# Optimization experiments

Hardware: AMD Instinct MI355X
Metric: run time of the kernel (lower is better)

Reference implementation:

```python
import jax, jax.numpy as jnp
import numpy as np

N_MAPS = 6          # n: maps per class (5 kernels + 1 text)
N_CLASSES = 2       # len(text_classify)
RATIO = 3
LAMBDA = 0.7
EPS = 1e-4
NEG_INF = -1e30


def setup_inputs() -> dict:
    key = jax.random.key(0)
    k1, k2, k3 = jax.random.split(key, 3)
    B, C, H, W = 8, N_CLASSES * N_MAPS, 640, 640
    outputs = jax.random.normal(k1, (B, C, H, W), dtype=jnp.float32)
    labels = jax.random.uniform(k2, (B, C, H, W), dtype=jnp.float32)
    training_mask = jax.random.uniform(k3, (B, 1, H, W), dtype=jnp.float32)
    return {"outputs": outputs, "labels": labels, "training_mask": training_mask}


def _dice_loss(pred, target, mask):
    # pred/target: (B, HW) or (B, K, HW); mask broadcastable. sums over last axis.
    p = jax.nn.sigmoid(pred) * mask
    t = target * mask
    a = jnp.sum(p * t, axis=-1)
    b = jnp.sum(p * p, axis=-1) + EPS
    c = jnp.sum(t * t, axis=-1) + EPS
    return 1.0 - 2.0 * a / (b + c)


def _ohem_single(score, gt, tm):
    # score/gt/tm: (H, W). Returns float32 (H, W) selection mask.
    pos_num = jnp.sum((gt > 0.5) & (tm > 0.5))
    neg = gt <= 0.5
    neg_total = jnp.sum(neg)
    neg_num = jnp.minimum(pos_num * RATIO, neg_total)
    # descending sort of negative-position scores
    neg_sorted = -jnp.sort(-jnp.where(neg, score, NEG_INF).ravel())
    thr = neg_sorted[jnp.clip(neg_num - 1, 0, score.size - 1)]
    sel = ((score >= thr) | (gt > 0.5)) & (tm > 0.5)
    fallback = (pos_num == 0) | (neg_num == 0)
    return jnp.where(fallback, tm, sel.astype(jnp.float32))


def reference(outputs, labels, training_mask):
    B, C, H, W = outputs.shape
    tm = training_mask[:, 0]  # (B, H, W)
    text_losses, kernel_losses, class_losses = [], [], []
    for i in range(N_CLASSES):
        texts = outputs[:, (i + 1) * N_MAPS - 1]                 # (B, H, W)
        kernels = outputs[:, i * N_MAPS:(i + 1) * N_MAPS - 1]    # (B, K, H, W)
        gt_texts = labels[:, (i + 1) * N_MAPS - 1]
        gt_kernels = labels[:, i * N_MAPS:(i + 1) * N_MAPS - 1]
        # OHEM mask (detached in original via numpy round-trip)
        sel_text = jax.lax.stop_gradient(jax.vmap(_ohem_single)(texts, gt_texts, tm))
        loss_text = _dice_loss(texts.reshape(B, -1), gt_texts.reshape(B, -1),
                               sel_text.reshape(B, -1))  # (B,)
        # kernel mask: (sigmoid(texts) > 0.5) & (tm > 0.5), detached
        sel_k = jax.lax.stop_gradient(
            ((jax.nn.sigmoid(texts) > 0.5) & (tm > 0.5)).astype(jnp.float32))
        K = gt_kernels.shape[1]
        loss_kernels = _dice_loss(kernels.reshape(B, K, -1),
                                  gt_kernels.reshape(B, K, -1),
                                  sel_k.reshape(B, 1, -1))  # (B, K) per-kernel losses
        loss_kernels = jnp.mean(loss_kernels, axis=1)  # mean over kernels -> (B,)
        lt = jnp.mean(loss_text)      # reduction='mean'
        lk = jnp.mean(loss_kernels)
        loss = LAMBDA * lt + (1.0 - LAMBDA) * lk
        text_losses.append(lt)
        kernel_losses.append(lk)
        class_losses.append(loss)
    muti_class_loss_avg = jnp.mean(jnp.stack(class_losses))
    text_loss_avg = jnp.mean(jnp.stack(text_losses))
    kernel_loss_avg = jnp.mean(jnp.stack(kernel_losses))
    # stacked as (3,): [muti_class_loss_avg, text_loss_avg, kernel_loss_avg]
    return jnp.stack([muti_class_loss_avg, text_loss_avg, kernel_loss_avg])
```

## Files before the change

### kernel.cpp

```cpp
#include <hip/hip_runtime.h>

#define HW 409600
#define NCH 12

#define OFF_TACC   0
#define OFF_KACC   256
#define OFF_POS    2048
#define OFF_NEG    2112
#define OFF_DONE   2176
#define OFF_FB     2240
#define OFF_NEGNUM 2304
#define OFF_MAXNK  2368
#define OFF_SEL1   2432
#define OFF_KREM1  2496
#define OFF_SEL2   2560
#define OFF_KREM2  2624
#define OFF_THR    2688
#define OFF_HA     4096
#define OFF_HB     (OFF_HA + 16*2048*4)
#define OFF_HC     (OFF_HB + 16*2048*4)
#define OFF_META_END (OFF_HC + 16*1024*4)
#define OFF_MASK   ((OFF_META_END + 255) & ~255)

__device__ __forceinline__ unsigned flipkey(float x){
  unsigned b = __float_as_uint(x);
  return (b & 0x80000000u) ? ~b : (b | 0x80000000u);
}
__device__ __forceinline__ float unflip(unsigned u){
  unsigned b = (u & 0x80000000u) ? (u ^ 0x80000000u) : ~u;
  return __uint_as_float(b);
}

__global__ __launch_bounds__(256) void k_count(
    const float* __restrict__ outputs, const float* __restrict__ labels,
    const float* __restrict__ tmask, unsigned char* __restrict__ maskb,
    unsigned* __restrict__ posA, unsigned* __restrict__ negA,
    unsigned* __restrict__ maxnkA)
{
  int img = blockIdx.x / 100;
  int blk = blockIdx.x % 100;
  int ci = img >> 3, bi = img & 7;
  const float* tp = outputs + (size_t)(bi*NCH + ci*6 + 5)*HW;
  const float* gp = labels  + (size_t)(bi*NCH + ci*6 + 5)*HW;
  const float* mp = tmask   + (size_t)bi*HW;
  int base = blk*4096 + (int)threadIdx.x*4;

  float4 tv0 = *(const float4*)(tp+base);
  float4 tv1 = *(const float4*)(tp+base+1024);
  float4 tv2 = *(const float4*)(tp+base+2048);
  float4 tv3 = *(const float4*)(tp+base+3072);
  float4 gv0 = *(const float4*)(gp+base);
  float4 gv1 = *(const float4*)(gp+base+1024);
  float4 gv2 = *(const float4*)(gp+base+2048);
  float4 gv3 = *(const float4*)(gp+base+3072);
  float4 mv0 = *(const float4*)(mp+base);
  float4 mv1 = *(const float4*)(mp+base+1024);
  float4 mv2 = *(const float4*)(mp+base+2048);
  float4 mv3 = *(const float4*)(mp+base+3072);

  float tt[16]={tv0.x,tv0.y,tv0.z,tv0.w, tv1.x,tv1.y,tv1.z,tv1.w,
                tv2.x,tv2.y,tv2.z,tv2.w, tv3.x,tv3.y,tv3.z,tv3.w};
  float gg[16]={gv0.x,gv0.y,gv0.z,gv0.w, gv1.x,gv1.y,gv1.z,gv1.w,
                gv2.x,gv2.y,gv2.z,gv2.w, gv3.x,gv3.y,gv3.z,gv3.w};
  float mm[16]={mv0.x,mv0.y,mv0.z,mv0.w, mv1.x,mv1.y,mv1.z,mv1.w,
                mv2.x,mv2.y,mv2.z,mv2.w, mv3.x,mv3.y,mv3.z,mv3.w};

  unsigned pos=0, neg=0, mn=0xFFFFFFFFu;
  unsigned char mb[16];
  #pragma unroll
  for (int c=0;c<16;c++){
    bool isneg = (gg[c] <= 0.5f);
    bool tpos  = (mm[c] > 0.5f);
    pos += (unsigned)((!isneg) && tpos);
    neg += (unsigned)isneg;
    mb[c] = (unsigned char)((((tt[c] > 0.0f) && tpos) ? 1u : 0u) |
                            (tpos ? 2u : 0u) | (isneg ? 4u : 0u));
    if (isneg){ unsigned k = flipkey(tt[c]); mn = (k<mn)?k:mn; }
  }
  unsigned char* mw = maskb + (size_t)img*HW + base;
  *(uchar4*)(mw)      = make_uchar4(mb[0],mb[1],mb[2],mb[3]);
  *(uchar4*)(mw+1024) = make_uchar4(mb[4],mb[5],mb[6],mb[7]);
  *(uchar4*)(mw+2048) = make_uchar4(mb[8],mb[9],mb[10],mb[11]);
  *(uchar4*)(mw+3072) = make_uchar4(mb[12],mb[13],mb[14],mb[15]);

  #pragma unroll
  for (int o=32;o;o>>=1){
    pos += __shfl_down(pos,o,64);
    neg += __shfl_down(neg,o,64);
    unsigned om = __shfl_down(mn,o,64); mn = (om<mn)?om:mn;
  }
  __shared__ unsigned sp[4], sn[4], sm[4];
  int wv = threadIdx.x >> 6, ln = threadIdx.x & 63;
  if (ln==0){ sp[wv]=pos; sn[wv]=neg; sm[wv]=mn; }
  __syncthreads();
  if (threadIdx.x==0){
    unsigned m01 = (sm[0]<sm[1])?sm[0]:sm[1];
    unsigned m23 = (sm[2]<sm[3])?sm[2]:sm[3];
    unsigned m = (m01<m23)?m01:m23;
    atomicAdd(&posA[img], sp[0]+sp[1]+sp[2]+sp[3]);
    atomicAdd(&negA[img], sn[0]+sn[1]+sn[2]+sn[3]);
    atomicMax(&maxnkA[img], ~m);
  }
}

__global__ void k_decide(
    const unsigned* __restrict__ posA, const unsigned* __restrict__ negA,
    const unsigned* __restrict__ maxnkA, unsigned* __restrict__ doneA,
    unsigned* __restrict__ fbA, unsigned* __restrict__ negnumA,
    float* __restrict__ thrA)
{
  int img = threadIdx.x;
  if (img >= 16) return;
  unsigned pos = posA[img], negt = negA[img];
  unsigned p3 = pos*3u;
  unsigned negnum = (p3 < negt) ? p3 : negt;
  if (pos==0u || negnum==0u){
    doneA[img]=1u; fbA[img]=1u; negnumA[img]=1u; thrA[img]=0.0f;
  } else if (negnum == negt){
    doneA[img]=1u; fbA[img]=0u; negnumA[img]=negnum;
    thrA[img] = unflip(~maxnkA[img]);
  } else {
    doneA[img]=0u; fbA[img]=0u; negnumA[img]=negnum; thrA[img]=0.0f;
  }
}


__global__ __launch_bounds__(256) void k_hista(
    const float* __restrict__ outputs, const unsigned char* __restrict__ maskb,
    const unsigned* __restrict__ doneA, unsigned* __restrict__ histA)
{
  int img = blockIdx.x / 50;
  if (doneA[img]) return;
  int blk = blockIdx.x % 50;
  int ci = img>>3, bi = img&7;
  const float* tp = outputs + (size_t)(bi*NCH + ci*6 + 5)*HW;
  const unsigned char* mk = maskb + (size_t)img*HW;
  __shared__ unsigned lh[2048];
  for (int j=threadIdx.x; j<2048; j+=256) lh[j]=0u;
  __syncthreads();
  #pragma unroll
  for (int it=0; it<8; it++){
    int px = blk*8192 + it*1024 + (int)threadIdx.x*4;
    float4 tv = *(const float4*)(tp+px);
    uchar4 mq = *(const uchar4*)(mk+px);
    float tt[4]={tv.x,tv.y,tv.z,tv.w};
    unsigned char ma[4]={mq.x,mq.y,mq.z,mq.w};
    #pragma unroll
    for (int c=0;c<4;c++)
      if (ma[c] & 4) atomicAdd(&lh[flipkey(tt[c]) >> 21], 1u);
  }
  __syncthreads();
  unsigned* gh = histA + (size_t)img*2048u;
  for (int j=threadIdx.x; j<2048; j+=256){
    unsigned v = lh[j];
    if (v) atomicAdd(&gh[j], v);
  }
}

template<int NB>
__device__ void scan_desc(const unsigned* h, unsigned k, unsigned* selOut, unsigned* kremOut)
{
  const int PER = NB/256;
  int t = threadIdx.x;
  unsigned s=0;
  #pragma unroll
  for (int j=0;j<PER;j++) s += h[t*PER+j];
  __shared__ unsigned cs[256];
  cs[t]=s; __syncthreads();
  if (t==0){
    unsigned cum=0, ch=0, kin=k;
    for (int c=255;c>=0;c--){
      if (cum + cs[c] >= k){ ch=(unsigned)c; kin=k-cum; break; }
      cum += cs[c];
    }
    unsigned cum2=0, sel=ch*PER, kr=1;
    for (int x=PER-1;x>=0;x--){
      unsigned v = h[ch*PER+x];
      cum2 += v;
      if (cum2 >= kin){ sel=ch*PER+(unsigned)x; kr = kin - (cum2 - v); break; }
    }
    *selOut = sel; *kremOut = kr;
  }
}

__global__ __launch_bounds__(256) void k_scan_a(
    const unsigned* __restrict__ histA, const unsigned* __restrict__ doneA,
    const unsigned* __restrict__ negnumA, unsigned* __restrict__ sel1A,
    unsigned* __restrict__ krem1A)
{
  int img = blockIdx.x;
  if (doneA[img]) return;
  scan_desc<2048>(histA + (size_t)img*2048u, negnumA[img], &sel1A[img], &krem1A[img]);
}

__global__ __launch_bounds__(256) void k_histb(
    const float* __restrict__ outputs, const unsigned char* __restrict__ maskb,
    const unsigned* __restrict__ sel1A, const unsigned* __restrict__ doneA,
    unsigned* __restrict__ histB)
{
  int img = blockIdx.x / 50;
  if (doneA[img]) return;
  int blk = blockIdx.x % 50;
  int ci = img>>3, bi = img&7;
  unsigned sel1 = sel1A[img];
  const float* tp = outputs + (size_t)(bi*NCH + ci*6 + 5)*HW;
  const unsigned char* mk = maskb + (size_t)img*HW;
  __shared__ unsigned lh[2048];
  for (int j=threadIdx.x; j<2048; j+=256) lh[j]=0u;
  __syncthreads();
  #pragma unroll
  for (int it=0; it<8; it++){
    int px = blk*8192 + it*1024 + (int)threadIdx.x*4;
    float4 tv = *(const float4*)(tp+px);
    uchar4 mq = *(const uchar4*)(mk+px);
    float tt[4]={tv.x,tv.y,tv.z,tv.w};
    unsigned char ma[4]={mq.x,mq.y,mq.z,mq.w};
    #pragma unroll
    for (int c=0;c<4;c++){
      if (ma[c] & 4){
        unsigned key = flipkey(tt[c]);
        if ((key>>21) == sel1) atomicAdd(&lh[(key>>10) & 0x7FFu], 1u);
      }
    }
  }
  __syncthreads();
  unsigned* gh = histB + (size_t)img*2048u;
  for (int j=threadIdx.x; j<2048; j+=256){
    unsigned v = lh[j];
    if (v) atomicAdd(&gh[j], v);
  }
}

__global__ __launch_bounds__(256) void k_scan_b(
    const unsigned* __restrict__ histB, const unsigned* __restrict__ krem1A,
    const unsigned* __restrict__ doneA, unsigned* __restrict__ sel2A,
    unsigned* __restrict__ krem2A)
{
  int img = blockIdx.x;
  if (doneA[img]) return;
  scan_desc<2048>(histB + (size_t)img*2048u, krem1A[img], &sel2A[img], &krem2A[img]);
}

__global__ __launch_bounds__(256) void k_histc(
    const float* __restrict__ outputs, const unsigned char* __restrict__ maskb,
    const unsigned* __restrict__ sel1A, const unsigned* __restrict__ sel2A,
    const unsigned* __restrict__ doneA, unsigned* __restrict__ histC)
{
  int img = blockIdx.x / 50;
  if (doneA[img]) return;
  int blk = blockIdx.x % 50;
  int ci = img>>3, bi = img&7;
  unsigned p22 = (sel1A[img]<<11) | sel2A[img];
  const float* tp = outputs + (size_t)(bi*NCH + ci*6 + 5)*HW;
  const unsigned char* mk = maskb + (size_t)img*HW;
  __shared__ unsigned lh[1024];
  for (int j=threadIdx.x; j<1024; j+=256) lh[j]=0u;
  __syncthreads();
  #pragma unroll
  for (int it=0; it<8; it++){
    int px = blk*8192 + it*1024 + (int)threadIdx.x*4;
    float4 tv = *(const float4*)(tp+px);
    uchar4 mq = *(const uchar4*)(mk+px);
    float tt[4]={tv.x,tv.y,tv.z,tv.w};
    unsigned char ma[4]={mq.x,mq.y,mq.z,mq.w};
    #pragma unroll
    for (int c=0;c<4;c++){
      if (ma[c] & 4){
        unsigned key = flipkey(tt[c]);
        if ((key>>10) == p22) atomicAdd(&lh[key & 0x3FFu], 1u);
      }
    }
  }
  __syncthreads();
  unsigned* gh = histC + (size_t)img*1024u;
  for (int j=threadIdx.x; j<1024; j+=256){
    unsigned v = lh[j];
    if (v) atomicAdd(&gh[j], v);
  }
}

__global__ __launch_bounds__(256) void k_scan_c(
    const unsigned* __restrict__ histC, const unsigned* __restrict__ sel1A,
    const unsigned* __restrict__ sel2A, const unsigned* __restrict__ krem2A,
    const unsigned* __restrict__ doneA, float* __restrict__ thrA)
{
  int img = blockIdx.x;
  if (doneA[img]) return;
  __shared__ unsigned sel3, kr;
  scan_desc<1024>(histC + (size_t)img*1024u, krem2A[img], &sel3, &kr);
  __syncthreads();
  if (threadIdx.x==0){
    unsigned key = (sel1A[img]<<21) | (sel2A[img]<<10) | sel3;
    thrA[img] = unflip(key);
  }
}

__global__ __launch_bounds__(256) void k_dice(
    const float* __restrict__ outputs, const float* __restrict__ labels,
    const float* __restrict__ tmask, const unsigned char* __restrict__ maskb,
    const unsigned* __restrict__ fbA, const float* __restrict__ thrA,
    float* __restrict__ tacc, float* __restrict__ kacc)
{
  int cimg = blockIdx.x / 50;
  int blk  = blockIdx.x % 50;
  int img = cimg / 6, j = cimg % 6;
  int ci = img>>3, bi = img&7;
  const float* pp_ = outputs + (size_t)(bi*NCH + ci*6 + j)*HW;
  const float* gp  = labels  + (size_t)(bi*NCH + ci*6 + j)*HW;
  const unsigned char* mk = maskb + (size_t)img*HW;
  const float* tmp = tmask + (size_t)bi*HW;
  bool istext = (j==5);
  bool fb = istext && (fbA[img] != 0u);
  float thr = istext ? thrA[img] : 0.0f;
  float sa=0.f, sb=0.f, sc=0.f;
  #pragma unroll
  for (int half=0; half<2; half++){
    int base = blk*8192 + half*4096 + (int)threadIdx.x*4;
    float4 pv0 = *(const float4*)(pp_+base);
    float4 pv1 = *(const float4*)(pp_+base+1024);
    float4 pv2 = *(const float4*)(pp_+base+2048);
    float4 pv3 = *(const float4*)(pp_+base+3072);
    float4 gv0 = *(const float4*)(gp+base);
    float4 gv1 = *(const float4*)(gp+base+1024);
    float4 gv2 = *(const float4*)(gp+base+2048);
    float4 gv3 = *(const float4*)(gp+base+3072);
    uchar4 mq0 = *(const uchar4*)(mk+base);
    uchar4 mq1 = *(const uchar4*)(mk+base+1024);
    uchar4 mq2 = *(const uchar4*)(mk+base+2048);
    uchar4 mq3 = *(const uchar4*)(mk+base+3072);
    float pa[16]={pv0.x,pv0.y,pv0.z,pv0.w, pv1.x,pv1.y,pv1.z,pv1.w,
                  pv2.x,pv2.y,pv2.z,pv2.w, pv3.x,pv3.y,pv3.z,pv3.w};
    float ga[16]={gv0.x,gv0.y,gv0.z,gv0.w, gv1.x,gv1.y,gv1.z,gv1.w,
                  gv2.x,gv2.y,gv2.z,gv2.w, gv3.x,gv3.y,gv3.z,gv3.w};
    unsigned char ma[16]={mq0.x,mq0.y,mq0.z,mq0.w, mq1.x,mq1.y,mq1.z,mq1.w,
                          mq2.x,mq2.y,mq2.z,mq2.w, mq3.x,mq3.y,mq3.z,mq3.w};
    float ta[16];
    if (fb){
      float4 t0=*(const float4*)(tmp+base),   t1=*(const float4*)(tmp+base+1024);
      float4 t2=*(const float4*)(tmp+base+2048), t3=*(const float4*)(tmp+base+3072);
      ta[0]=t0.x;ta[1]=t0.y;ta[2]=t0.z;ta[3]=t0.w; ta[4]=t1.x;ta[5]=t1.y;ta[6]=t1.z;ta[7]=t1.w;
      ta[8]=t2.x;ta[9]=t2.y;ta[10]=t2.z;ta[11]=t2.w; ta[12]=t3.x;ta[13]=t3.y;ta[14]=t3.z;ta[15]=t3.w;
    }
    #pragma unroll
    for (int c=0;c<16;c++){
      float m;
      if (istext){
        if (fb) m = ta[c];
        else    m = (((pa[c] >= thr) || (ga[c] > 0.5f)) && (ma[c] & 2)) ? 1.0f : 0.0f;
      } else {
        m = (ma[c] & 1) ? 1.0f : 0.0f;
      }
      float p = __fdividef(1.0f, 1.0f + __expf(-pa[c])) * m;
      float tt = ga[c]*m;
      sa += p*tt; sb += p*p; sc += tt*tt;
    }
  }
  #pragma unroll
  for (int o=32;o;o>>=1){
    sa += __shfl_down(sa,o,64); sb += __shfl_down(sb,o,64); sc += __shfl_down(sc,o,64);
  }
  __shared__ float ra[4], rb[4], rc[4];
  int wv = threadIdx.x>>6, ln = threadIdx.x&63;
  if (ln==0){ ra[wv]=sa; rb[wv]=sb; rc[wv]=sc; }
  __syncthreads();
  if (threadIdx.x==0){
    float A=ra[0]+ra[1]+ra[2]+ra[3];
    float Bs=rb[0]+rb[1]+rb[2]+rb[3];
    float Cs=rc[0]+rc[1]+rc[2]+rc[3];
    float* acc = istext ? (tacc + img*3) : (kacc + (img*5 + j)*3);
    atomicAdd(acc+0, A); atomicAdd(acc+1, Bs); atomicAdd(acc+2, Cs);
  }
}

__global__ void k_final(const float* __restrict__ tacc, const float* __restrict__ kacc,
                        float* __restrict__ out)
{
  if (blockIdx.x==0 && threadIdx.x==0){
    const float EPSF = 1e-4f;
    float ltA[2], lkA[2];
    for (int i=0;i<2;i++){
      float lt=0.f;
      for (int b=0;b<8;b++){
        int img=i*8+b;
        float a=tacc[img*3], p2=tacc[img*3+1]+EPSF, t2=tacc[img*3+2]+EPSF;
        lt += 1.f - 2.f*a/(p2+t2);
      }
      lt *= 0.125f;
      float lk=0.f;
      for (int b=0;b<8;b++) for (int k=0;k<5;k++){
        int idx=((i*8+b)*5+k)*3;
        float a=kacc[idx], p2=kacc[idx+1]+EPSF, t2=kacc[idx+2]+EPSF;
        lk += 1.f - 2.f*a/(p2+t2);
      }
      lk /= 40.f;
      ltA[i]=lt; lkA[i]=lk;
    }
    float l0 = 0.7f*ltA[0] + 0.3f*lkA[0];
    float l1 = 0.7f*ltA[1] + 0.3f*lkA[1];
    out[0]=0.5f*(l0+l1);
    out[1]=0.5f*(ltA[0]+ltA[1]);
    out[2]=0.5f*(lkA[0]+lkA[1]);
  }
}

extern "C" void kernel_launch(void* const* d_in, const int* in_sizes, int n_in,
                              void* d_out, int out_size, void* d_ws, size_t ws_size,
                              hipStream_t stream)
{
  const float* outputs = (const float*)d_in[0];
  const float* labels  = (const float*)d_in[1];
  const float* tmask   = (const float*)d_in[2];
  float* out = (float*)d_out;
  char* ws = (char*)d_ws;
  float* tacc      = (float*)(ws + OFF_TACC);
  float* kacc      = (float*)(ws + OFF_KACC);
  unsigned* posA   = (unsigned*)(ws + OFF_POS);
  unsigned* negA   = (unsigned*)(ws + OFF_NEG);
  unsigned* doneA  = (unsigned*)(ws + OFF_DONE);
  unsigned* fbA    = (unsigned*)(ws + OFF_FB);
  unsigned* negnumA= (unsigned*)(ws + OFF_NEGNUM);
  unsigned* maxnkA = (unsigned*)(ws + OFF_MAXNK);
  unsigned* sel1A  = (unsigned*)(ws + OFF_SEL1);
  unsigned* krem1A = (unsigned*)(ws + OFF_KREM1);
  unsigned* sel2A  = (unsigned*)(ws + OFF_SEL2);
  unsigned* krem2A = (unsigned*)(ws + OFF_KREM2);
  float* thrA      = (float*)(ws + OFF_THR);
  unsigned* histA  = (unsigned*)(ws + OFF_HA);
  unsigned* histB  = (unsigned*)(ws + OFF_HB);
  unsigned* histC  = (unsigned*)(ws + OFF_HC);
  unsigned char* maskb = (unsigned char*)(ws + OFF_MASK);

  hipMemsetAsync(ws, 0, OFF_META_END, stream);
  k_count <<<1600,256,0,stream>>>(outputs, labels, tmask, maskb, posA, negA, maxnkA);
  k_decide<<<1,64,0,stream>>>(posA, negA, maxnkA, doneA, fbA, negnumA, thrA);
  k_hista <<<800,256,0,stream>>>(outputs, maskb, doneA, histA);
  k_scan_a<<<16,256,0,stream>>>(histA, doneA, negnumA, sel1A, krem1A);
  k_histb <<<800,256,0,stream>>>(outputs, maskb, sel1A, doneA, histB);
  k_scan_b<<<16,256,0,stream>>>(histB, krem1A, doneA, sel2A, krem2A);
  k_histc <<<800,256,0,stream>>>(outputs, maskb, sel1A, sel2A, doneA, histC);
  k_scan_c<<<16,256,0,stream>>>(histC, sel1A, sel2A, krem2A, doneA, thrA);
  k_dice  <<<4800,256,0,stream>>>(outputs, labels, tmask, maskb, fbA, thrA, tacc, kacc);
  k_final <<<1,64,0,stream>>>(tacc, kacc, out);
}
```

Before: 371.3 us.

## Fuse counting and kernel dice into single pass with precomputed text fast/fallback sums

Merges the count kernel and the kernel-map dice reduction into one pass over all six channels per class. It also accumulates text dice sums for both the fallback and the all-negatives-selected case, so k_decide can finalize those images without a second text pass. The text dice kernel now runs only for images needing the histogram threshold. Pos/neg counts move to float atomics, which adds register pressure and more shuffle reductions but reduces total memory traffic.

```diff
diff --git a/kernel.cpp b/kernel.cpp
--- a/kernel.cpp
+++ b/kernel.cpp
@@ -5,17 +5,17 @@
 
 #define OFF_TACC   0
 #define OFF_KACC   256
-#define OFF_POS    2048
-#define OFF_NEG    2112
-#define OFF_DONE   2176
-#define OFF_FB     2240
-#define OFF_NEGNUM 2304
-#define OFF_MAXNK  2368
-#define OFF_SEL1   2432
-#define OFF_KREM1  2496
-#define OFF_SEL2   2560
-#define OFF_KREM2  2624
-#define OFF_THR    2688
+#define OFF_TFAST  1280
+#define OFF_TFB    1536
+#define OFF_POSF   1792
+#define OFF_NEGF   1856
+#define OFF_DONE   1920
+#define OFF_NEGNUM 1984
+#define OFF_SEL1   2048
+#define OFF_KREM1  2112
+#define OFF_SEL2   2176
+#define OFF_KREM2  2240
+#define OFF_THR    2304
 #define OFF_HA     4096
 #define OFF_HB     (OFF_HA + 16*2048*4)
 #define OFF_HC     (OFF_HB + 16*2048*4)
@@ -31,96 +31,146 @@
   return __uint_as_float(b);
 }
 
-__global__ __launch_bounds__(256) void k_count(
+__device__ __forceinline__ float sigm(float x){
+  return __fdividef(1.0f, 1.0f + __expf(-x));
+}
+
+__global__ __launch_bounds__(256) void k_main(
     const float* __restrict__ outputs, const float* __restrict__ labels,
     const float* __restrict__ tmask, unsigned char* __restrict__ maskb,
-    unsigned* __restrict__ posA, unsigned* __restrict__ negA,
-    unsigned* __restrict__ maxnkA)
-{
-  int img = blockIdx.x / 100;
-  int blk = blockIdx.x % 100;
+    float* __restrict__ posF, float* __restrict__ negF,
+    float* __restrict__ tfastA, float* __restrict__ tfbA,
+    float* __restrict__ kaccA)
+{
+  int img = blockIdx.x / 200;
+  int blk = blockIdx.x % 200;
   int ci = img >> 3, bi = img & 7;
-  const float* tp = outputs + (size_t)(bi*NCH + ci*6 + 5)*HW;
-  const float* gp = labels  + (size_t)(bi*NCH + ci*6 + 5)*HW;
+  const float* ob = outputs + (size_t)(bi*NCH + ci*6)*HW;
+  const float* lb = labels  + (size_t)(bi*NCH + ci*6)*HW;
   const float* mp = tmask   + (size_t)bi*HW;
-  int base = blk*4096 + (int)threadIdx.x*4;
-
-  float4 tv0 = *(const float4*)(tp+base);
-  float4 tv1 = *(const float4*)(tp+base+1024);
-  float4 tv2 = *(const float4*)(tp+base+2048);
-  float4 tv3 = *(const float4*)(tp+base+3072);
-  float4 gv0 = *(const float4*)(gp+base);
-  float4 gv1 = *(const float4*)(gp+base+1024);
-  float4 gv2 = *(const float4*)(gp+base+2048);
-  float4 gv3 = *(const float4*)(gp+base+3072);
-  float4 mv0 = *(const float4*)(mp+base);
-  float4 mv1 = *(const float4*)(mp+base+1024);
-  float4 mv2 = *(const float4*)(mp+base+2048);
-  float4 mv3 = *(const float4*)(mp+base+3072);
-
-  float tt[16]={tv0.x,tv0.y,tv0.z,tv0.w, tv1.x,tv1.y,tv1.z,tv1.w,
-                tv2.x,tv2.y,tv2.z,tv2.w, tv3.x,tv3.y,tv3.z,tv3.w};
-  float gg[16]={gv0.x,gv0.y,gv0.z,gv0.w, gv1.x,gv1.y,gv1.z,gv1.w,
-                gv2.x,gv2.y,gv2.z,gv2.w, gv3.x,gv3.y,gv3.z,gv3.w};
-  float mm[16]={mv0.x,mv0.y,mv0.z,mv0.w, mv1.x,mv1.y,mv1.z,mv1.w,
-                mv2.x,mv2.y,mv2.z,mv2.w, mv3.x,mv3.y,mv3.z,mv3.w};
-
-  unsigned pos=0, neg=0, mn=0xFFFFFFFFu;
-  unsigned char mb[16];
-  #pragma unroll
-  for (int c=0;c<16;c++){
-    bool isneg = (gg[c] <= 0.5f);
-    bool tpos  = (mm[c] > 0.5f);
-    pos += (unsigned)((!isneg) && tpos);
-    neg += (unsigned)isneg;
-    mb[c] = (unsigned char)((((tt[c] > 0.0f) && tpos) ? 1u : 0u) |
-                            (tpos ? 2u : 0u) | (isneg ? 4u : 0u));
-    if (isneg){ unsigned k = flipkey(tt[c]); mn = (k<mn)?k:mn; }
-  }
-  unsigned char* mw = maskb + (size_t)img*HW + base;
-  *(uchar4*)(mw)      = make_uchar4(mb[0],mb[1],mb[2],mb[3]);
-  *(uchar4*)(mw+1024) = make_uchar4(mb[4],mb[5],mb[6],mb[7]);
-  *(uchar4*)(mw+2048) = make_uchar4(mb[8],mb[9],mb[10],mb[11]);
-  *(uchar4*)(mw+3072) = make_uchar4(mb[12],mb[13],mb[14],mb[15]);
-
-  #pragma unroll
-  for (int o=32;o;o>>=1){
-    pos += __shfl_down(pos,o,64);
-    neg += __shfl_down(neg,o,64);
-    unsigned om = __shfl_down(mn,o,64); mn = (om<mn)?om:mn;
-  }
-  __shared__ unsigned sp[4], sn[4], sm[4];
+  unsigned char* mw = maskb + (size_t)img*HW;
+
+  float ka0=0,ka1=0,ka2=0,ka3=0,ka4=0;
+  float kb0=0,kb1=0,kb2=0,kb3=0,kb4=0;
+  float kc0=0,kc1=0,kc2=0,kc3=0,kc4=0;
+  float af=0,bf=0,cf=0;
+  float ab_=0,bb_=0,cb_=0;
+  unsigned pos=0, neg=0;
+
+  #pragma unroll
+  for (int it=0; it<2; it++){
+    int px = blk*2048 + it*1024 + (int)threadIdx.x*4;
+    float4 ov0 = *(const float4*)(ob + 0*HW + px);
+    float4 ov1 = *(const float4*)(ob + 1*HW + px);
+    float4 ov2 = *(const float4*)(ob + 2*HW + px);
+    float4 ov3 = *(const float4*)(ob + 3*HW + px);
+    float4 ov4 = *(const float4*)(ob + 4*HW + px);
+    float4 ov5 = *(const float4*)(ob + 5*HW + px);
+    float4 lv0 = *(const float4*)(lb + 0*HW + px);
+    float4 lv1 = *(const float4*)(lb + 1*HW + px);
+    float4 lv2 = *(const float4*)(lb + 2*HW + px);
+    float4 lv3 = *(const float4*)(lb + 3*HW + px);
+    float4 lv4 = *(const float4*)(lb + 4*HW + px);
+    float4 lv5 = *(const float4*)(lb + 5*HW + px);
+    float4 mv  = *(const float4*)(mp + px);
+
+    float oo[6][4] = {{ov0.x,ov0.y,ov0.z,ov0.w},{ov1.x,ov1.y,ov1.z,ov1.w},
+                      {ov2.x,ov2.y,ov2.z,ov2.w},{ov3.x,ov3.y,ov3.z,ov3.w},
+                      {ov4.x,ov4.y,ov4.z,ov4.w},{ov5.x,ov5.y,ov5.z,ov5.w}};
+    float ll[6][4] = {{lv0.x,lv0.y,lv0.z,lv0.w},{lv1.x,lv1.y,lv1.z,lv1.w},
+                      {lv2.x,lv2.y,lv2.z,lv2.w},{lv3.x,lv3.y,lv3.z,lv3.w},
+                      {lv4.x,lv4.y,lv4.z,lv4.w},{lv5.x,lv5.y,lv5.z,lv5.w}};
+    float tmv[4] = {mv.x,mv.y,mv.z,mv.w};
+    unsigned char mby[4];
+
+    #pragma unroll
+    for (int c=0;c<4;c++){
+      float t  = oo[5][c];
+      float g  = ll[5][c];
+      float tm = tmv[c];
+      bool tpos  = (tm > 0.5f);
+      bool isneg = (g <= 0.5f);
+      bool selk  = (t > 0.0f) && tpos;
+      pos += (unsigned)((!isneg) && tpos);
+      neg += (unsigned)isneg;
+      mby[c] = (unsigned char)((selk?1u:0u)|(tpos?2u:0u)|(isneg?4u:0u));
+
+      float s5 = sigm(t);
+      float mf = tpos ? 1.0f : 0.0f;
+      af += mf * (s5*g);
+      bf += mf * (s5*s5);
+      cf += mf * (g*g);
+      float pfb = s5*tm, tfb = g*tm;
+      ab_ += pfb*tfb; bb_ += pfb*pfb; cb_ += tfb*tfb;
+      float mk = selk ? 1.0f : 0.0f;
+      {
+        float s, l;
+        s = sigm(oo[0][c]); l = ll[0][c];
+        ka0 += mk*(s*l); kb0 += mk*(s*s); kc0 += mk*(l*l);
+        s = sigm(oo[1][c]); l = ll[1][c];
+        ka1 += mk*(s*l); kb1 += mk*(s*s); kc1 += mk*(l*l);
+        s = sigm(oo[2][c]); l = ll[2][c];
+        ka2 += mk*(s*l); kb2 += mk*(s*s); kc2 += mk*(l*l);
+        s = sigm(oo[3][c]); l = ll[3][c];
+        ka3 += mk*(s*l); kb3 += mk*(s*s); kc3 += mk*(l*l);
+        s = sigm(oo[4][c]); l = ll[4][c];
+        ka4 += mk*(s*l); kb4 += mk*(s*s); kc4 += mk*(l*l);
+      }
+    }
+    *(uchar4*)(mw + px) = make_uchar4(mby[0],mby[1],mby[2],mby[3]);
+  }
+
+  float red[23] = {af,bf,cf, ab_,bb_,cb_,
+                   ka0,kb0,kc0, ka1,kb1,kc1, ka2,kb2,kc2,
+                   ka3,kb3,kc3, ka4,kb4,kc4,
+                   (float)pos, (float)neg};
+  #pragma unroll
+  for (int k=0;k<23;k++){
+    #pragma unroll
+    for (int o=32;o;o>>=1) red[k] += __shfl_down(red[k],o,64);
+  }
+  __shared__ float sred[4][23];
   int wv = threadIdx.x >> 6, ln = threadIdx.x & 63;
-  if (ln==0){ sp[wv]=pos; sn[wv]=neg; sm[wv]=mn; }
-  __syncthreads();
-  if (threadIdx.x==0){
-    unsigned m01 = (sm[0]<sm[1])?sm[0]:sm[1];
-    unsigned m23 = (sm[2]<sm[3])?sm[2]:sm[3];
-    unsigned m = (m01<m23)?m01:m23;
-    atomicAdd(&posA[img], sp[0]+sp[1]+sp[2]+sp[3]);
-    atomicAdd(&negA[img], sn[0]+sn[1]+sn[2]+sn[3]);
-    atomicMax(&maxnkA[img], ~m);
+  if (ln==0){
+    #pragma unroll
+    for (int k=0;k<23;k++) sred[wv][k] = red[k];
+  }
+  __syncthreads();
+  int t = threadIdx.x;
+  if (t < 23){
+    float v = sred[0][t]+sred[1][t]+sred[2][t]+sred[3][t];
+    float* dst;
+    if      (t < 3)  dst = tfastA + img*3 + t;
+    else if (t < 6)  dst = tfbA   + img*3 + (t-3);
+    else if (t < 21) dst = kaccA  + img*15 + (t-6);
+    else if (t ==21) dst = posF + img;
+    else             dst = negF + img;
+    atomicAdd(dst, v);
   }
 }
 
 __global__ void k_decide(
-    const unsigned* __restrict__ posA, const unsigned* __restrict__ negA,
-    const unsigned* __restrict__ maxnkA, unsigned* __restrict__ doneA,
-    unsigned* __restrict__ fbA, unsigned* __restrict__ negnumA,
-    float* __restrict__ thrA)
+    const float* __restrict__ posF, const float* __restrict__ negF,
+    const float* __restrict__ tfastA, const float* __restrict__ tfbA,
+    float* __restrict__ tacc, unsigned* __restrict__ doneA,
+    unsigned* __restrict__ negnumA, float* __restrict__ thrA)
 {
   int img = threadIdx.x;
   if (img >= 16) return;
-  unsigned pos = posA[img], negt = negA[img];
-  unsigned p3 = pos*3u;
-  unsigned negnum = (p3 < negt) ? p3 : negt;
-  if (pos==0u || negnum==0u){
-    doneA[img]=1u; fbA[img]=1u; negnumA[img]=1u; thrA[img]=0.0f;
-  } else if (negnum == negt){
-    doneA[img]=1u; fbA[img]=0u; negnumA[img]=negnum;
-    thrA[img] = unflip(~maxnkA[img]);
+  float pos = posF[img], negt = negF[img];
+  float nn = fminf(pos*3.0f, negt);
+  bool fb   = (pos == 0.0f) || (nn == 0.0f);
+  bool fast = (!fb) && (nn == negt);
+  thrA[img] = 0.0f;
+  if (fb || fast){
+    doneA[img] = 1u; negnumA[img] = 1u;
+    const float* src = fb ? (tfbA + img*3) : (tfastA + img*3);
+    tacc[img*3+0] = src[0];
+    tacc[img*3+1] = src[1];
+    tacc[img*3+2] = src[2];
   } else {
-    doneA[img]=0u; fbA[img]=0u; negnumA[img]=negnum; thrA[img]=0.0f;
+    doneA[img] = 0u;
+    negnumA[img] = (unsigned)(nn + 0.5f);
   }
 }
 
@@ -295,31 +345,27 @@
   }
 }
 
-__global__ __launch_bounds__(256) void k_dice(
+__global__ __launch_bounds__(256) void k_dtext(
     const float* __restrict__ outputs, const float* __restrict__ labels,
-    const float* __restrict__ tmask, const unsigned char* __restrict__ maskb,
-    const unsigned* __restrict__ fbA, const float* __restrict__ thrA,
-    float* __restrict__ tacc, float* __restrict__ kacc)
-{
-  int cimg = blockIdx.x / 50;
-  int blk  = blockIdx.x % 50;
-  int img = cimg / 6, j = cimg % 6;
+    const unsigned char* __restrict__ maskb, const unsigned* __restrict__ doneA,
+    const float* __restrict__ thrA, float* __restrict__ tacc)
+{
+  int img = blockIdx.x / 50;
+  if (doneA[img]) return;
+  int blk = blockIdx.x % 50;
   int ci = img>>3, bi = img&7;
-  const float* pp_ = outputs + (size_t)(bi*NCH + ci*6 + j)*HW;
-  const float* gp  = labels  + (size_t)(bi*NCH + ci*6 + j)*HW;
+  const float* tp = outputs + (size_t)(bi*NCH + ci*6 + 5)*HW;
+  const float* gp = labels  + (size_t)(bi*NCH + ci*6 + 5)*HW;
   const unsigned char* mk = maskb + (size_t)img*HW;
-  const float* tmp = tmask + (size_t)bi*HW;
-  bool istext = (j==5);
-  bool fb = istext && (fbA[img] != 0u);
-  float thr = istext ? thrA[img] : 0.0f;
+  float thr = thrA[img];
   float sa=0.f, sb=0.f, sc=0.f;
   #pragma unroll
   for (int half=0; half<2; half++){
     int base = blk*8192 + half*4096 + (int)threadIdx.x*4;
-    float4 pv0 = *(const float4*)(pp_+base);
-    float4 pv1 = *(const float4*)(pp_+base+1024);
-    float4 pv2 = *(const float4*)(pp_+base+2048);
-    float4 pv3 = *(const float4*)(pp_+base+3072);
+    float4 pv0 = *(const float4*)(tp+base);
+    float4 pv1 = *(const float4*)(tp+base+1024);
+    float4 pv2 = *(const float4*)(tp+base+2048);
+    float4 pv3 = *(const float4*)(tp+base+3072);
     float4 gv0 = *(const float4*)(gp+base);
     float4 gv1 = *(const float4*)(gp+base+1024);
     float4 gv2 = *(const float4*)(gp+base+2048);
@@ -334,23 +380,10 @@
                   gv2.x,gv2.y,gv2.z,gv2.w, gv3.x,gv3.y,gv3.z,gv3.w};
     unsigned char ma[16]={mq0.x,mq0.y,mq0.z,mq0.w, mq1.x,mq1.y,mq1.z,mq1.w,
                           mq2.x,mq2.y,mq2.z,mq2.w, mq3.x,mq3.y,mq3.z,mq3.w};
-    float ta[16];
-    if (fb){
-      float4 t0=*(const float4*)(tmp+base),   t1=*(const float4*)(tmp+base+1024);
-      float4 t2=*(const float4*)(tmp+base+2048), t3=*(const float4*)(tmp+base+3072);
-      ta[0]=t0.x;ta[1]=t0.y;ta[2]=t0.z;ta[3]=t0.w; ta[4]=t1.x;ta[5]=t1.y;ta[6]=t1.z;ta[7]=t1.w;
-      ta[8]=t2.x;ta[9]=t2.y;ta[10]=t2.z;ta[11]=t2.w; ta[12]=t3.x;ta[13]=t3.y;ta[14]=t3.z;ta[15]=t3.w;
-    }
     #pragma unroll
     for (int c=0;c<16;c++){
-      float m;
-      if (istext){
-        if (fb) m = ta[c];
-        else    m = (((pa[c] >= thr) || (ga[c] > 0.5f)) && (ma[c] & 2)) ? 1.0f : 0.0f;
-      } else {
-        m = (ma[c] & 1) ? 1.0f : 0.0f;
-      }
-      float p = __fdividef(1.0f, 1.0f + __expf(-pa[c])) * m;
+      float m = (((pa[c] >= thr) || (ga[c] > 0.5f)) && (ma[c] & 2)) ? 1.0f : 0.0f;
+      float p = sigm(pa[c]) * m;
       float tt = ga[c]*m;
       sa += p*tt; sb += p*p; sc += tt*tt;
     }
@@ -364,11 +397,10 @@
   if (ln==0){ ra[wv]=sa; rb[wv]=sb; rc[wv]=sc; }
   __syncthreads();
   if (threadIdx.x==0){
-    float A=ra[0]+ra[1]+ra[2]+ra[3];
-    float Bs=rb[0]+rb[1]+rb[2]+rb[3];
-    float Cs=rc[0]+rc[1]+rc[2]+rc[3];
-    float* acc = istext ? (tacc + img*3) : (kacc + (img*5 + j)*3);
-    atomicAdd(acc+0, A); atomicAdd(acc+1, Bs); atomicAdd(acc+2, Cs);
+    float* acc = tacc + img*3;
+    atomicAdd(acc+0, ra[0]+ra[1]+ra[2]+ra[3]);
+    atomicAdd(acc+1, rb[0]+rb[1]+rb[2]+rb[3]);
+    atomicAdd(acc+2, rc[0]+rc[1]+rc[2]+rc[3]);
   }
 }
 
@@ -414,12 +446,12 @@
   char* ws = (char*)d_ws;
   float* tacc      = (float*)(ws + OFF_TACC);
   float* kacc      = (float*)(ws + OFF_KACC);
-  unsigned* posA   = (unsigned*)(ws + OFF_POS);
-  unsigned* negA   = (unsigned*)(ws + OFF_NEG);
+  float* tfastA    = (float*)(ws + OFF_TFAST);
+  float* tfbA      = (float*)(ws + OFF_TFB);
+  float* posF      = (float*)(ws + OFF_POSF);
+  float* negF      = (float*)(ws + OFF_NEGF);
   unsigned* doneA  = (unsigned*)(ws + OFF_DONE);
-  unsigned* fbA    = (unsigned*)(ws + OFF_FB);
   unsigned* negnumA= (unsigned*)(ws + OFF_NEGNUM);
-  unsigned* maxnkA = (unsigned*)(ws + OFF_MAXNK);
   unsigned* sel1A  = (unsigned*)(ws + OFF_SEL1);
   unsigned* krem1A = (unsigned*)(ws + OFF_KREM1);
   unsigned* sel2A  = (unsigned*)(ws + OFF_SEL2);
@@ -431,14 +463,15 @@
   unsigned char* maskb = (unsigned char*)(ws + OFF_MASK);
 
   hipMemsetAsync(ws, 0, OFF_META_END, stream);
-  k_count <<<1600,256,0,stream>>>(outputs, labels, tmask, maskb, posA, negA, maxnkA);
-  k_decide<<<1,64,0,stream>>>(posA, negA, maxnkA, doneA, fbA, negnumA, thrA);
+  k_main  <<<3200,256,0,stream>>>(outputs, labels, tmask, maskb, posF, negF,
+                                  tfastA, tfbA, kacc);
+  k_decide<<<1,64,0,stream>>>(posF, negF, tfastA, tfbA, tacc, doneA, negnumA, thrA);
   k_hista <<<800,256,0,stream>>>(outputs, maskb, doneA, histA);
   k_scan_a<<<16,256,0,stream>>>(histA, doneA, negnumA, sel1A, krem1A);
   k_histb <<<800,256,0,stream>>>(outputs, maskb, sel1A, doneA, histB);
   k_scan_b<<<16,256,0,stream>>>(histB, krem1A, doneA, sel2A, krem2A);
   k_histc <<<800,256,0,stream>>>(outputs, maskb, sel1A, sel2A, doneA, histC);
   k_scan_c<<<16,256,0,stream>>>(histC, sel1A, sel2A, krem2A, doneA, thrA);
-  k_dice  <<<4800,256,0,stream>>>(outputs, labels, tmask, maskb, fbA, thrA, tacc, kacc);
+  k_dtext <<<800,256,0,stream>>>(outputs, labels, maskb, doneA, thrA, tacc);
   k_final <<<1,64,0,stream>>>(tacc, kacc, out);
 }
```

After: 353.3 us. 4.8% less time.
